# Optimization experiments

Measured on AMD Instinct MI355X. Metric: run time of the kernel, lower is better.

Reference implementation:

```python
import jax, jax.numpy as jnp
import numpy as np

B, L, F, H, HDE, E, V, MH, MW, TOUT = 64, 2, 512, 512, 512, 512, 94, 6, 40, 30
V2 = V + 2          # vocab + START/END + NULL slots
T = TOUT + 2        # decode steps
HW = MH * MW
START = V + 1
END = V + 1


def setup_inputs() -> dict:
    key = jax.random.key(0)
    ks = jax.random.split(key, 20)
    s = 0.05  # weight scale for numerical stability
    n = lambda k, shape: jax.random.normal(k, shape, jnp.float32) * s
    d = {}
    d['conv_f'] = jax.random.normal(ks[0], (B, F, MH, MW), jnp.float32)
    d['target'] = jax.random.randint(ks[1], (B, TOUT), 0, 95, dtype=jnp.int32)
    d['w_ih_en'] = n(ks[2], (L, 4 * H, F))
    d['w_hh_en'] = n(ks[3], (L, 4 * H, H))
    d['b_ih_en'] = n(ks[4], (L, 4 * H))
    d['b_hh_en'] = n(ks[5], (L, 4 * H))
    d['embed_w'] = n(ks[6], (V2, H))
    d['w_ih_de'] = n(ks[7], (L, 4 * HDE, H))
    d['w_hh_de'] = n(ks[8], (L, 4 * HDE, HDE))
    d['b_ih_de'] = n(ks[9], (L, 4 * HDE))
    d['b_hh_de'] = n(ks[10], (L, 4 * HDE))
    d['att_wh'] = n(ks[11], (E, HDE))
    d['att_bh'] = n(ks[12], (E,))
    d['att_conv_w'] = n(ks[13], (E, F, 3, 3))
    d['att_conv_b'] = n(ks[14], (E,))
    d['att_wv'] = n(ks[15], (1, E))
    d['att_bv'] = n(ks[16], (1,))
    d['out_w'] = n(ks[17], (V2, HDE + F))
    d['out_b'] = n(ks[18], (V2,))
    return d


def _lstm_cell(x, h, c, wih, whh, bih, bhh):
    # PyTorch gate order: i, f, g, o
    g = x @ wih.T + h @ whh.T + bih + bhh
    i, f, gg, o = jnp.split(g, 4, axis=-1)
    c_new = jax.nn.sigmoid(f) * c + jax.nn.sigmoid(i) * jnp.tanh(gg)
    h_new = jax.nn.sigmoid(o) * jnp.tanh(c_new)
    return h_new, c_new


def _forward(conv_f, target, w_ih_en, w_hh_en, b_ih_en, b_hh_en, embed_w,
             w_ih_de, w_hh_de, b_ih_de, b_hh_de, att_wh, att_bh,
             att_conv_w, att_conv_b, att_wv, att_bv, out_w, out_b):
    # ---- encoder: maxpool over full height, then 2-layer LSTM over width ----
    x_seq = jnp.max(conv_f, axis=2).transpose(2, 0, 1)  # [W, B, F]

    def enc_step(carry, xt):
        h, c = carry
        inp = xt
        hs, cs = [], []
        for l in range(L):
            hl, cl = _lstm_cell(inp, h[l], c[l], w_ih_en[l], w_hh_en[l],
                                b_ih_en[l], b_hh_en[l])
            inp = hl
            hs.append(hl); cs.append(cl)
        return (jnp.stack(hs), jnp.stack(cs)), inp

    z = jnp.zeros((L, B, H), conv_f.dtype)
    _, enc_out = jax.lax.scan(enc_step, (z, z), x_seq)
    holistic = enc_out[-1]  # [B, H]

    # ---- attention: conv_f embedding computed ONCE (invariant across steps) ----
    xe = jax.lax.conv_general_dilated(
        conv_f, att_conv_w, (1, 1), 'SAME',
        dimension_numbers=('NCHW', 'OIHW', 'NCHW')) + att_conv_b[None, :, None, None]
    x_em = xe.reshape(B, E, HW).transpose(0, 2, 1)       # [B, HW, E]
    cf_flat = conv_f.reshape(B, F, HW).transpose(0, 2, 1)  # [B, HW, F]

    # ---- decoder inputs: t=0 holistic, t>=1 embed(gt_with_start[:, t-1]) ----
    gt = jnp.concatenate(
        [jnp.full((B, 1), START, dtype=target.dtype), target], axis=1)  # [B, T-1]
    xs = jnp.concatenate([holistic[None], embed_w[gt.T]], axis=0)  # [T, B, H]

    def dec_step(carry, xt):
        h, c = carry
        inp = xt
        hs, cs = [], []
        for l in range(L):
            hl, cl = _lstm_cell(inp, h[l], c[l], w_ih_de[l], w_hh_de[l],
                                b_ih_de[l], b_hh_de[l])
            inp = hl
            hs.append(hl); cs.append(cl)
        hlast = inp  # [B, HDE]
        g_em = hlast @ att_wh.T + att_bh                    # [B, E]
        feat = jnp.tanh(x_em + g_em[:, None, :])            # [B, HW, E] (dropout=identity)
        e = feat @ att_wv[0] + att_bv[0]                    # [B, HW]
        alpha = jax.nn.softmax(e, axis=-1)
        att = jnp.einsum('bw,bwf->bf', alpha, cf_flat)      # [B, F]
        logits = jnp.concatenate([hlast, att], axis=-1) @ out_w.T + out_b
        scores = jax.nn.log_softmax(logits, axis=-1)        # [B, V2]
        return (jnp.stack(hs), jnp.stack(cs)), scores

    zd = jnp.zeros((B, HDE), conv_f.dtype)
    z0 = jnp.stack([zd] * L)
    _, out_tbv = jax.lax.scan(dec_step, (z0, z0), xs)  # [T, B, V2]
    out = out_tbv.transpose(1, 0, 2)                    # [B, T, V2]

    # ---- build l_target: [0, target..., 0] with first padding 0 -> END ----
    l_target = jnp.zeros((B, T), jnp.int32).at[:, 1:-1].set(target)
    j = jnp.argmax(l_target[:, 1:] == 0, axis=1) + 1  # first zero at col>=1 (always exists)
    l_target = l_target.at[jnp.arange(B), j].set(END)

    # ---- masked NLL loss ----
    lt = l_target.reshape(-1)
    nll = -out.reshape(-1, V2)[jnp.arange(B * T), lt]
    mask = (lt != 0).astype(out.dtype)
    return jnp.sum(nll * mask) / jnp.sum(mask)


def reference(conv_f, target, w_ih_en, w_hh_en, b_ih_en, b_hh_en, embed_w,
              w_ih_de, w_hh_de, b_ih_de, b_hh_de, att_wh, att_bh,
              att_conv_w, att_conv_b, att_wv, att_bv, out_w, out_b):
    return _forward(conv_f, target, w_ih_en, w_hh_en, b_ih_en, b_hh_en, embed_w,
                    w_ih_de, w_hh_de, b_ih_de, b_hh_de, att_wh, att_bh,
                    att_conv_w, att_conv_b, att_wv, att_bv, out_w, out_b)
```

## Files before the change

kernel.cpp:

```cpp
#include <hip/hip_runtime.h>

typedef __fp16 f16;
typedef __fp16 f16x4 __attribute__((ext_vector_type(4)));
typedef __fp16 f16x8 __attribute__((ext_vector_type(8)));
typedef float  f32x4 __attribute__((ext_vector_type(4)));
typedef unsigned long long ull;

#define DEV static __device__ __forceinline__

DEV f32x4 mfma16(f16x4 a, f16x4 b, f32x4 c) {
  return __builtin_amdgcn_mfma_f32_16x16x16f16(a, b, c, 0, 0, 0);
}
DEV f16x4 lo4(f16x8 v) { return __builtin_shufflevector(v, v, 0, 1, 2, 3); }
DEV f16x4 hi4(f16x8 v) { return __builtin_shufflevector(v, v, 4, 5, 6, 7); }
DEV float sigf(float x) { return 1.f / (1.f + __expf(-x)); }
DEV float tanh_(float x) { float e = __expf(2.f * x); return 1.f - 2.f / (e + 1.f); }

union U8 { float4 f4; float2 f2[2]; };
union H2 { unsigned u; f16 h[2]; };
union H4 { ull u; f16 h[4]; f16x4 v; };

#define HB 32768

DEV ull ldU(const ull* p) {
  return __hip_atomic_load(p, __ATOMIC_RELAXED, __HIP_MEMORY_SCOPE_AGENT);
}
DEV unsigned ldF(const unsigned* p) {
  return __hip_atomic_load(p, __ATOMIC_RELAXED, __HIP_MEMORY_SCOPE_AGENT);
}
DEV void stU32(unsigned* p, unsigned v) {
  __hip_atomic_store(p, v, __ATOMIC_RELAXED, __HIP_MEMORY_SCOPE_AGENT);
}
DEV void stU64(ull* p, ull v) {
  __hip_atomic_store(p, v, __ATOMIC_RELAXED, __HIP_MEMORY_SCOPE_AGENT);
}

DEV void wait8(const unsigned* line, unsigned tgt) {
  if (threadIdx.x < 8)
    while (ldF(line + threadIdx.x * 16) < tgt) {}
  __syncthreads();
}

DEV void signalDone(unsigned* line, int slot) {
  asm volatile("s_waitcnt vmcnt(0)" ::: "memory");
  __syncthreads();
  if (threadIdx.x == 0)
    __hip_atomic_fetch_add(line + slot * 16, 1u, __ATOMIC_RELAXED, __HIP_MEMORY_SCOPE_AGENT);
}

DEV void stageRow(const f16* __restrict__ s, f16* __restrict__ dstRow, int ch) {
  U8 u0, u1;
  u0.f4 = *(const float4*)s;
  u1.f4 = *(const float4*)(s + 8);
  *(float2*)(dstRow +  0 + ch * 4) = u0.f2[0];
  *(float2*)(dstRow + 16 + ch * 4) = u0.f2[1];
  *(float2*)(dstRow + 32 + ch * 4) = u1.f2[0];
  *(float2*)(dstRow + 48 + ch * 4) = u1.f2[1];
}

DEV void stageAp(const f16* __restrict__ rowSrc, f16 (*A)[64][72], int tid) {
  int ch = tid & 3;
  const f16* s = rowSrc + ch * 16;
#pragma unroll
  for (int c = 0; c < 8; ++c)
    stageRow(s + c * 64, &A[c][tid >> 2][0], ch);
}

DEV void stageAu(const ull* __restrict__ srcU, f16 (*A)[64][72], int tid) {
  int row = tid >> 2, ch = tid & 3;
  const ull* s = srcU + row * 128 + ch * 4;
#pragma unroll
  for (int c = 0; c < 8; ++c) {
    ull d0 = ldU(s + c * 16 + 0);
    ull d1 = ldU(s + c * 16 + 1);
    ull d2 = ldU(s + c * 16 + 2);
    ull d3 = ldU(s + c * 16 + 3);
    f16* d = &A[c][row][0];
    *(ull*)(d +  0 + ch * 4) = d0;
    *(ull*)(d + 16 + ch * 4) = d1;
    *(ull*)(d + 32 + ch * 4) = d2;
    *(ull*)(d + 48 + ch * 4) = d3;
  }
}

DEV void kloop32(const f16 (*Wt)[32][72], const f16 (*A)[64][72],
                 int mh, int ns, int m16, int g4, f32x4 acc[2]) {
#pragma unroll
  for (int c = 0; c < 8; ++c) {
#pragma unroll
    for (int half = 0; half < 2; ++half) {
      f16x8 bf = *(const f16x8*)&Wt[c][ns * 16 + m16][g4 * 16 + half * 8];
      f16x4 bl = lo4(bf), bh = hi4(bf);
#pragma unroll
      for (int mt = 0; mt < 2; ++mt) {
        f16x8 af = *(const f16x8*)&A[c][mh * 32 + mt * 16 + m16][g4 * 16 + half * 8];
        acc[mt] = mfma16(lo4(af), bl, acc[mt]);
        acc[mt] = mfma16(hi4(af), bh, acc[mt]);
      }
    }
  }
}

DEV void kloop64(const f16* Wg, const f16 (*A)[64][72],
                 int nsG, int m16, int g4, f32x4 acc[4]) {
#pragma unroll
  for (int c = 0; c < 8; ++c) {
#pragma unroll
    for (int half = 0; half < 2; ++half) {
      f16x8 bf = *(const f16x8*)&Wg[((size_t)(c * 64 + nsG * 16 + m16)) * 72 + g4 * 16 + half * 8];
      f16x4 bl = lo4(bf), bh = hi4(bf);
#pragma unroll
      for (int mt = 0; mt < 4; ++mt) {
        f16x8 af = *(const f16x8*)&A[c][mt * 16 + m16][g4 * 16 + half * 8];
        acc[mt] = mfma16(lo4(af), bl, acc[mt]);
        acc[mt] = mfma16(hi4(af), bh, acc[mt]);
      }
    }
  }
}

DEV void convTile(char* smem, int tile, const f16* __restrict__ cfT,
                  const f16* __restrict__ wc9, const float* __restrict__ cb,
                  f16* __restrict__ xemH) {
  f16 (*At)[40] = (f16(*)[40])smem;
  f16 (*Bt)[40] = (f16(*)[40])(smem + 19200);
  const int t = threadIdx.x, lane = t & 63, w = t >> 6;
  const int b = tile >> 2, eb = (tile & 3) * 128;
  const int m16 = lane & 15, g4 = lane >> 4;
  f32x4 acc[15][2] = {};

  for (int kr = 0; kr < 9; ++kr) {
    int dh = kr / 3 - 1, dw = kr % 3 - 1;
    for (int f0 = 0; f0 < 512; f0 += 32) {
      __syncthreads();
      if (t < 240) {
        int hh = t / 40 + dh, ww = t % 40 + dw;
        if (hh >= 0 && hh < 6 && ww >= 0 && ww < 40) {
          const f16* s = cfT + ((size_t)(b * 240 + hh * 40 + ww) * 512 + f0);
          U8 u0, u1, u2, u3;
          u0.f4 = *(const float4*)s;        u1.f4 = *(const float4*)(s + 8);
          u2.f4 = *(const float4*)(s + 16); u3.f4 = *(const float4*)(s + 24);
          *(float2*)&At[t][ 0] = u0.f2[0];
          *(float2*)&At[t][ 8] = u0.f2[1];
          *(float2*)&At[t][16] = u1.f2[0];
          *(float2*)&At[t][24] = u1.f2[1];
          *(float2*)&At[t][ 4] = u2.f2[0];
          *(float2*)&At[t][12] = u2.f2[1];
          *(float2*)&At[t][20] = u3.f2[0];
          *(float2*)&At[t][28] = u3.f2[1];
        } else {
          float2 z = make_float2(0.f, 0.f);
          *(float2*)&At[t][ 0] = z; *(float2*)&At[t][ 8] = z;
          *(float2*)&At[t][16] = z; *(float2*)&At[t][24] = z;
          *(float2*)&At[t][ 4] = z; *(float2*)&At[t][12] = z;
          *(float2*)&At[t][20] = z; *(float2*)&At[t][28] = z;
        }
      }
      {
        int n = t >> 1, ch = t & 1;
        const f16* s = wc9 + (size_t)(eb + n) * 4608 + kr * 512 + f0 + ch * 16;
        U8 u0, u1;
        u0.f4 = *(const float4*)s; u1.f4 = *(const float4*)(s + 8);
        *(float2*)&Bt[n][ 0 + ch * 4] = u0.f2[0];
        *(float2*)&Bt[n][ 8 + ch * 4] = u0.f2[1];
        *(float2*)&Bt[n][16 + ch * 4] = u1.f2[0];
        *(float2*)&Bt[n][24 + ch * 4] = u1.f2[1];
      }
      __syncthreads();
      f16x8 b0 = *(const f16x8*)&Bt[w * 32 + m16][g4 * 8];
      f16x8 b1v = *(const f16x8*)&Bt[w * 32 + 16 + m16][g4 * 8];
      f16x4 b0l = lo4(b0), b0h = hi4(b0), b1l = lo4(b1v), b1h = hi4(b1v);
#pragma unroll
      for (int mt = 0; mt < 15; ++mt) {
        f16x8 af = *(const f16x8*)&At[mt * 16 + m16][g4 * 8];
        f16x4 al = lo4(af), ah = hi4(af);
        acc[mt][0] = mfma16(al, b0l, acc[mt][0]);
        acc[mt][1] = mfma16(al, b1l, acc[mt][1]);
        acc[mt][0] = mfma16(ah, b0h, acc[mt][0]);
        acc[mt][1] = mfma16(ah, b1h, acc[mt][1]);
      }
    }
  }
#pragma unroll
  for (int nt = 0; nt < 2; ++nt) {
    int e = eb + w * 32 + nt * 16 + m16;
    float bias = cb[e];
#pragma unroll
    for (int mt = 0; mt < 15; ++mt)
#pragma unroll
      for (int r = 0; r < 4; ++r) {
        int p = mt * 16 + g4 * 4 + r;
        xemH[((size_t)(b * 240 + p)) * 512 + e] = (f16)(acc[mt][nt][r] + bias);
      }
  }
}


__global__ void k_convW(const float* __restrict__ s0, const float* __restrict__ s1,
                        const float* __restrict__ s2, const float* __restrict__ s3,
                        f16* __restrict__ d0, f16* __restrict__ d1,
                        f16* __restrict__ d2, f16* __restrict__ d3) {
  int i = blockIdx.x * 256 + threadIdx.x;
  int sel = i >> 19, j = i & 524287;
  const float* s = sel == 0 ? s0 : sel == 1 ? s1 : sel == 2 ? s2 : s3;
  f16* d = sel == 0 ? d0 : sel == 1 ? d1 : sel == 2 ? d2 : d3;
  float4 v = ((const float4*)s)[j];
  f16x4 o = { (f16)v.x, (f16)v.y, (f16)v.z, (f16)v.w };
  *(f16x4*)(d + (size_t)j * 4) = o;
}

__global__ void k_convS(const float* __restrict__ awhS, const float* __restrict__ embS,
                        const float* __restrict__ outwS,
                        f16* __restrict__ awhD, f16* __restrict__ embD,
                        f16* __restrict__ outwD) {
  int i = blockIdx.x * 256 + threadIdx.x;
  const float* s; f16* d; int j;
  if (i < 65536) { s = awhS; d = awhD; j = i; }
  else if (i < 65536 + 12288) { s = embS; d = embD; j = i - 65536; }
  else if (i < 65536 + 12288 + 24576) { s = outwS; d = outwD; j = i - 65536 - 12288; }
  else return;
  float4 v = ((const float4*)s)[j];
  f16x4 o = { (f16)v.x, (f16)v.y, (f16)v.z, (f16)v.w };
  *(f16x4*)(d + (size_t)j * 4) = o;
}

__global__ __launch_bounds__(256) void k_wc9(const float* __restrict__ src, f16* __restrict__ dst) {
  __shared__ float s[4608];
  const int e = blockIdx.x, tid = threadIdx.x;
  for (int i = tid; i < 4608; i += 256) s[i] = src[(size_t)e * 4608 + i];
  __syncthreads();
  for (int j = tid; j < 4608; j += 256) {
    int rr = j >> 9, f = j & 511;
    dst[(size_t)e * 4608 + j] = (f16)s[f * 9 + rr];
  }
}

__global__ __launch_bounds__(256) void k_cfmx(
    const float* __restrict__ cf, f16* __restrict__ cfT, f16* __restrict__ xseq)
{
  __shared__ float sT[64][244];
  const int tid = threadIdx.x;
  const int f0 = blockIdx.x * 64, b = blockIdx.y;
  const float* src = cf + ((size_t)b * 512 + f0) * 240;
  for (int i = tid; i < 3840; i += 256) {
    float4 v = ((const float4*)src)[i];
    int fl = i / 60, pc = (i % 60) * 4;
    sT[fl][pc] = v.x; sT[fl][pc + 1] = v.y; sT[fl][pc + 2] = v.z; sT[fl][pc + 3] = v.w;
  }
  __syncthreads();
  if (tid < 240) {
    int p = tid;
    f16* drow = cfT + ((size_t)b * 240 + p) * 512 + f0;
#pragma unroll
    for (int j = 0; j < 8; ++j) {
      f16x8 o;
#pragma unroll
      for (int k = 0; k < 8; ++k) o[k] = (f16)sT[j * 8 + k][p];
      *(f16x8*)(drow + j * 8) = o;
    }
  }
  {
    int fl = tid >> 2, wq = tid & 3;
#pragma unroll
    for (int wi = 0; wi < 10; ++wi) {
      int w = wq * 10 + wi;
      float m = sT[fl][w];
#pragma unroll
      for (int h = 1; h < 6; ++h) m = fmaxf(m, sT[fl][h * 40 + w]);
      xseq[((size_t)w * 64 + b) * 512 + f0 + fl] = (f16)m;
    }
  }
}

__global__ void k_zero(unsigned* p0, unsigned* p1, unsigned* p2,
                       unsigned* p3, unsigned* p4, unsigned* p5) {
  int i = blockIdx.x * 256 + threadIdx.x;
  int sel = i >> 14, j = i & 16383;
  unsigned* p = sel == 0 ? p0 : sel == 1 ? p1 : sel == 2 ? p2 :
                sel == 3 ? p3 : sel == 4 ? p4 : p5;
  p[j] = 0;
}

__global__ __launch_bounds__(256) void k_gemmX(
    const f16* __restrict__ A, const f16* __restrict__ W,
    const float* __restrict__ b1, const float* __restrict__ b2,
    f16* __restrict__ C)
{
  __shared__ f16 At[64][72];
  __shared__ f16 Bt[64][72];
  const int t = threadIdx.x, lane = t & 63, g = t >> 6;
  f32x4 acc[4] = {};
  const int m16 = lane & 15, g4 = lane >> 4;
  const size_t arow0 = (size_t)blockIdx.x * 64;

  for (int k0 = 0; k0 < 512; k0 += 64) {
    __syncthreads();
    { int row = t >> 2, ch = t & 3;
      stageRow(A + (arow0 + row) * 512 + k0 + ch * 16, &At[row][0], ch); }
    { int row = t >> 2, ch = t & 3;
      stageRow(W + ((size_t)blockIdx.y * 64 + row) * 512 + k0 + ch * 16, &Bt[row][0], ch); }
    __syncthreads();
#pragma unroll
    for (int half = 0; half < 2; ++half) {
      f16x8 bf = *(const f16x8*)&Bt[g * 16 + m16][g4 * 16 + half * 8];
      f16x4 bl = lo4(bf), bh = hi4(bf);
#pragma unroll
      for (int mt = 0; mt < 4; ++mt) {
        f16x8 af = *(const f16x8*)&At[mt * 16 + m16][g4 * 16 + half * 8];
        acc[mt] = mfma16(lo4(af), bl, acc[mt]);
        acc[mt] = mfma16(hi4(af), bh, acc[mt]);
      }
    }
  }
  int e = blockIdx.y * 64 + g * 16 + m16;
  float bias = b1[e] + b2[e];
#pragma unroll
  for (int mt = 0; mt < 4; ++mt)
#pragma unroll
    for (int r = 0; r < 4; ++r)
      C[(arow0 + mt * 16 + g4 * 4 + r) * 2048 + e] = (f16)(acc[mt][r] + bias);
}

__global__ __launch_bounds__(256) void k_gemmXd(
    const f16* __restrict__ x_t0, const f16* __restrict__ emb, const int* __restrict__ tgt,
    const f16* __restrict__ W, const float* __restrict__ b1, const float* __restrict__ b2,
    f16* __restrict__ C)
{
  __shared__ f16 At[64][72];
  __shared__ f16 Bt[64][72];
  const int t = threadIdx.x, lane = t & 63, g = t >> 6;
  f32x4 acc[4] = {};
  const int m16 = lane & 15, g4 = lane >> 4;
  const int tt = blockIdx.x;
  const size_t arow0 = (size_t)tt * 64;
  const int row = t >> 2, ch = t & 3;
  const f16* rowSrc;
  if (tt == 0) rowSrc = x_t0 + (size_t)row * 512;
  else if (tt == 1) rowSrc = emb + (size_t)95 * 512;
  else { int tok = tgt[row * 30 + tt - 2]; rowSrc = emb + (size_t)tok * 512; }

  for (int k0 = 0; k0 < 512; k0 += 64) {
    __syncthreads();
    stageRow(rowSrc + k0 + ch * 16, &At[row][0], ch);
    stageRow(W + ((size_t)blockIdx.y * 64 + row) * 512 + k0 + ch * 16, &Bt[row][0], ch);
    __syncthreads();
#pragma unroll
    for (int half = 0; half < 2; ++half) {
      f16x8 bf = *(const f16x8*)&Bt[g * 16 + m16][g4 * 16 + half * 8];
      f16x4 bl = lo4(bf), bh = hi4(bf);
#pragma unroll
      for (int mt = 0; mt < 4; ++mt) {
        f16x8 af = *(const f16x8*)&At[mt * 16 + m16][g4 * 16 + half * 8];
        acc[mt] = mfma16(lo4(af), bl, acc[mt]);
        acc[mt] = mfma16(hi4(af), bh, acc[mt]);
      }
    }
  }
  int e = blockIdx.y * 64 + g * 16 + m16;
  float bias = b1[e] + b2[e];
#pragma unroll
  for (int mt = 0; mt < 4; ++mt)
#pragma unroll
    for (int r = 0; r < 4; ++r)
      C[(arow0 + mt * 16 + g4 * 4 + r) * 2048 + e] = (f16)(acc[mt][r] + bias);
}

__global__ __launch_bounds__(256, 1) void k_lstm(
    int T, int mode,
    const f16* __restrict__ G0, const f16* __restrict__ whh0,
    const f16* __restrict__ wih1, const f16* __restrict__ whh1,
    const float* __restrict__ bih1, const float* __restrict__ bhh1,
    f16* __restrict__ h0seq, f16* __restrict__ h1seq,
    unsigned* __restrict__ cnt,
    const f16* __restrict__ cfT, const f16* __restrict__ wc9,
    const float* __restrict__ cb, f16* __restrict__ xemH, int convBase,
    f16* __restrict__ X0de, const f16* __restrict__ wihD0,
    const float* __restrict__ bihD0, const float* __restrict__ bhhD0,
    const f16* __restrict__ emb, const int* __restrict__ tgt,
    const f16* __restrict__ awh, const float* __restrict__ gbias, f16* __restrict__ gAll)
{
  __shared__ __align__(16) char smem[147456];
  const int tid = threadIdx.x, lane = tid & 63, w = tid >> 6;
  const int m16 = lane & 15, g4 = lane >> 4;
  const int bid = blockIdx.x;

  if (bid < 32) {
    f16 (*sW)[64][72] = (f16(*)[64][72])smem;
    f16 (*sA)[64][72] = (f16(*)[64][72])(smem + 73728);
    float* sG = (float*)(smem + 73728);
    const int utile = bid;
    { int r = tid >> 2, ch = tid & 3;
      int grow = (r >> 4) * 512 + utile * 16 + (r & 15);
      for (int c = 0; c < 8; ++c)
        stageRow(whh0 + (size_t)grow * 512 + c * 64 + ch * 16, &sW[c][r][0], ch);
    }
    const int pb = tid >> 2, uq = tid & 3;
    float cst[4] = {0.f, 0.f, 0.f, 0.f};
    for (int t = 0; t < T; ++t) {
      if (t > 0) wait8(cnt + (size_t)(t - 1) * 128, 4);
      const f16* gpp = G0 + (size_t)(t * 64 + pb) * 2048 + utile * 16 + uq * 4;
      H4 gI, gF, gG, gO;
      gI.v = *(const f16x4*)(gpp);
      gF.v = *(const f16x4*)(gpp + 512);
      gG.v = *(const f16x4*)(gpp + 1024);
      gO.v = *(const f16x4*)(gpp + 1536);
      stageAu((const ull*)h0seq + (size_t)t * 8192, sA, tid);
      __syncthreads();
      f32x4 acc[4] = {};
      kloop64((const f16*)sW, sA, w, m16, g4, acc);
      __syncthreads();
#pragma unroll
      for (int mt = 0; mt < 4; ++mt)
#pragma unroll
        for (int r = 0; r < 4; ++r)
          sG[((size_t)w * 64 + mt * 16 + g4 * 4 + r) * 17 + m16] = acc[mt][r];
      __syncthreads();
      {
        H4 outp;
#pragma unroll
        for (int j = 0; j < 4; ++j) {
          int u = uq * 4 + j;
          float gi = sG[(0 * 64 + pb) * 17 + u] + (float)gI.h[j];
          float gf = sG[(1 * 64 + pb) * 17 + u] + (float)gF.h[j];
          float gg = sG[(2 * 64 + pb) * 17 + u] + (float)gG.h[j];
          float go = sG[(3 * 64 + pb) * 17 + u] + (float)gO.h[j];
          float cn = sigf(gf) * cst[j] + sigf(gi) * tanh_(gg);
          float hn = sigf(go) * tanh_(cn);
          cst[j] = cn;
          outp.h[j] = (f16)hn;
        }
        stU64((ull*)h0seq + (size_t)(t + 1) * 8192 + pb * 128 + utile * 4 + uq, outp.u);
      }
      signalDone(cnt + (size_t)t * 128, bid & 7);
    }
  } else if (bid < 96) {
    f16 (*sW2)[8][32][72] = (f16(*)[8][32][72])smem;
    f16 (*sA)[64][72] = (f16(*)[64][72])(smem + 73728);
    float* sG = (float*)(smem + 73728);
    const int utile = bid - 32;
    const int mh = w >> 1, ns = w & 1;
    { int mat = tid >> 7;
      int r = (tid >> 2) & 31, ch = tid & 3;
      int grow = (r >> 3) * 512 + utile * 8 + (r & 7);
      const f16* Wsrc = (mat == 0) ? wih1 : whh1;
      for (int c = 0; c < 8; ++c)
        stageRow(Wsrc + (size_t)grow * 512 + c * 64 + ch * 16, &sW2[mat][c][r][0], ch);
    }
    const int pb = tid >> 2, pup = tid & 3;
    float badd[4][2];
#pragma unroll
    for (int g = 0; g < 4; ++g)
#pragma unroll
      for (int j = 0; j < 2; ++j) {
        int rr = g * 512 + utile * 8 + pup * 2 + j;
        badd[g][j] = bih1[rr] + bhh1[rr];
      }
    float cst[2] = {0.f, 0.f};
    unsigned* line1 = cnt + (size_t)T * 128;
    for (int t = 0; t < T; ++t) {
      wait8(cnt + (size_t)t * 128, 4);
      stageAu((const ull*)h0seq + (size_t)(t + 1) * 8192, sA, tid);
      if (t > 0) wait8(line1 + (size_t)(t - 1) * 128, 8);
      else       __syncthreads();
      ull rg[8][4];
      { const ull* s1p = (const ull*)h1seq + (size_t)t * 8192 + (tid >> 2) * 128 + (tid & 3) * 4;
#pragma unroll
        for (int c = 0; c < 8; ++c)
#pragma unroll
          for (int q = 0; q < 4; ++q) rg[c][q] = ldU(s1p + c * 16 + q);
      }
      f32x4 acc[2] = {};
      kloop32(sW2[0], sA, mh, ns, m16, g4, acc);
      __syncthreads();
      { int row = tid >> 2, ch = tid & 3;
#pragma unroll
        for (int c = 0; c < 8; ++c) {
          f16* d = &sA[c][row][0];
          *(ull*)(d +  0 + ch * 4) = rg[c][0];
          *(ull*)(d + 16 + ch * 4) = rg[c][1];
          *(ull*)(d + 32 + ch * 4) = rg[c][2];
          *(ull*)(d + 48 + ch * 4) = rg[c][3];
        }
      }
      __syncthreads();
      kloop32(sW2[1], sA, mh, ns, m16, g4, acc);
      __syncthreads();
      { int nl = ns * 16 + m16;
#pragma unroll
        for (int mt = 0; mt < 2; ++mt)
#pragma unroll
          for (int r = 0; r < 4; ++r) {
            int b = mh * 32 + mt * 16 + g4 * 4 + r;
            sG[((nl >> 3) * 64 + b) * 9 + (nl & 7)] = acc[mt][r];
          }
      }
      __syncthreads();
      {
        H2 outp;
#pragma unroll
        for (int j = 0; j < 2; ++j) {
          int u = pup * 2 + j;
          float gi = sG[(0 * 64 + pb) * 9 + u] + badd[0][j];
          float gf = sG[(1 * 64 + pb) * 9 + u] + badd[1][j];
          float gg = sG[(2 * 64 + pb) * 9 + u] + badd[2][j];
          float go = sG[(3 * 64 + pb) * 9 + u] + badd[3][j];
          float cn = sigf(gf) * cst[j] + sigf(gi) * tanh_(gg);
          float hn = sigf(go) * tanh_(cn);
          cst[j] = cn;
          outp.h[j] = (f16)hn;
        }
        stU32((unsigned*)h1seq + (size_t)(t + 1) * 16384 + pb * 256 + utile * 4 + pup, outp.u);
      }
      signalDone(line1 + (size_t)t * 128, bid & 7);
    }
  } else if (bid < 224) {
    convTile(smem, convBase + bid - 96, cfT, wc9, cb, xemH);
  } else if (mode == 0) {
    const int rid = bid - 224;
    f16 (*sW)[64][72] = (f16(*)[64][72])smem;
    f16 (*sA)[64][72] = (f16(*)[64][72])(smem + 73728);
    { int r = tid >> 2, ch = tid & 3;
      for (int c = 0; c < 8; ++c)
        stageRow(wihD0 + (size_t)(rid * 64 + r) * 512 + c * 64 + ch * 16, &sW[c][r][0], ch);
    }
    const int e = rid * 64 + w * 16 + m16;
    const float bias_e = bihD0[e] + bhhD0[e];
    const int arow = tid >> 2;
    __syncthreads();
    for (int tt = 1; tt < 32; ++tt) {
      const f16* rowSrc = (tt == 1) ? emb + (size_t)95 * 512
                                    : emb + (size_t)tgt[arow * 30 + tt - 2] * 512;
      stageAp(rowSrc, sA, tid);
      __syncthreads();
      f32x4 acc[4] = {};
      kloop64((const f16*)sW, sA, w, m16, g4, acc);
      __syncthreads();
#pragma unroll
      for (int mt = 0; mt < 4; ++mt)
#pragma unroll
        for (int r = 0; r < 4; ++r)
          X0de[((size_t)tt * 64 + mt * 16 + g4 * 4 + r) * 2048 + e] = (f16)(acc[mt][r] + bias_e);
      __syncthreads();
    }
  } else {
    const int g = bid - 224;
    f16* sWg = (f16*)smem;
    f16 (*sA)[64][72] = (f16(*)[64][72])(smem + 73728);
    { int r = tid >> 2, ch = tid & 3;
      for (int c = 0; c < 8; ++c)
        stageRow(awh + (size_t)(g * 64 + r) * 512 + c * 64 + ch * 16,
                 sWg + ((size_t)(c * 64 + r)) * 72, ch);
    }
    const int e = g * 64 + w * 16 + m16;
    const float gb = gbias[e];
    __syncthreads();
    unsigned* line1 = cnt + (size_t)T * 128;
    for (int t = 0; t < T; ++t) {
      wait8(line1 + (size_t)t * 128, 8);
      stageAu((const ull*)h1seq + (size_t)(t + 1) * 8192, sA, tid);
      __syncthreads();
      f32x4 acc[4] = {};
      kloop64(sWg, sA, w, m16, g4, acc);
      __syncthreads();
#pragma unroll
      for (int mt = 0; mt < 4; ++mt)
#pragma unroll
        for (int r = 0; r < 4; ++r)
          gAll[(size_t)(t * 64 + mt * 16 + g4 * 4 + r) * 512 + e] = (f16)(acc[mt][r] + gb);
    }
  }
}


__global__ __launch_bounds__(256) void k_scoreAll(
    const f16* __restrict__ xemH, const f16* __restrict__ gAll,
    const float* __restrict__ wv, float* __restrict__ esc)
{
  __shared__ f16 sX[20][512];
  const int tid = threadIdx.x, lane = tid & 63, w = tid >> 6;
  const int tile = blockIdx.x, b = blockIdx.y;
  for (int i = tid; i < 20 * 64; i += 256) {
    int row = i >> 6, seg = i & 63;
    *(f16x8*)&sX[row][seg * 8] =
        *(const f16x8*)(xemH + ((size_t)(b * 240 + tile * 20 + row)) * 512 + seg * 8);
  }
  float w8[8];
  { const float4* wp = (const float4*)(wv + lane * 8);
    float4 wa = wp[0], wb = wp[1];
    w8[0] = wa.x; w8[1] = wa.y; w8[2] = wa.z; w8[3] = wa.w;
    w8[4] = wb.x; w8[5] = wb.y; w8[6] = wb.z; w8[7] = wb.w; }
  __syncthreads();
  for (int t = 0; t < 32; ++t) {
    f16x8 gv = *(const f16x8*)(gAll + ((size_t)(t * 64 + b)) * 512 + lane * 8);
    float g8[8];
#pragma unroll
    for (int j = 0; j < 8; ++j) g8[j] = (float)gv[j];
#pragma unroll
    for (int i = 0; i < 5; ++i) {
      int rr = i * 4 + w;
      f16x8 xv = *(const f16x8*)&sX[rr][lane * 8];
      float s = 0.f;
#pragma unroll
      for (int j = 0; j < 8; ++j) s += tanh_((float)xv[j] + g8[j]) * w8[j];
#pragma unroll
      for (int m = 32; m; m >>= 1) s += __shfl_xor(s, m);
      if (lane == 0) esc[((size_t)(t * 64 + b)) * 240 + tile * 20 + rr] = s;
    }
  }
}

__global__ __launch_bounds__(256) void k_smctx(
    const float* __restrict__ esc, const f16* __restrict__ cfT,
    const f16* __restrict__ h1seq, f16* __restrict__ ctx)
{
  __shared__ float aAl[8][240];
  const int tid = threadIdx.x, lane = tid & 63, w = tid >> 6;
  const int tq = blockIdx.x, b = blockIdx.y;
  for (int half = 0; half < 2; ++half) {
    int tt = w + half * 4;
    int t = tq * 8 + tt;
    const float* er = esc + ((size_t)(t * 64 + b)) * 240;
    float v[4];
    float mx = -1e30f;
#pragma unroll
    for (int q = 0; q < 4; ++q) {
      int p = lane + q * 64;
      v[q] = (p < 240) ? er[p] : -1e30f;
      mx = fmaxf(mx, v[q]);
    }
#pragma unroll
    for (int m = 32; m; m >>= 1) mx = fmaxf(mx, __shfl_xor(mx, m));
    float sum = 0.f;
#pragma unroll
    for (int q = 0; q < 4; ++q) { v[q] = __expf(v[q] - mx); sum += v[q]; }
#pragma unroll
    for (int m = 32; m; m >>= 1) sum += __shfl_xor(sum, m);
    float inv = 1.f / sum;
#pragma unroll
    for (int q = 0; q < 4; ++q) {
      int p = lane + q * 64;
      if (p < 240) aAl[tt][p] = v[q] * inv;
    }
  }
  __syncthreads();
  float acc[8][2] = {};
  const f16* cb = cfT + (size_t)b * 240 * 512;
  for (int p = 0; p < 240; ++p) {
    H2 cw; cw.u = *(const unsigned*)(cb + (size_t)p * 512 + tid * 2);
    float c0 = (float)cw.h[0], c1 = (float)cw.h[1];
#pragma unroll
    for (int tt = 0; tt < 8; ++tt) {
      float a = aAl[tt][p];
      acc[tt][0] += a * c0;
      acc[tt][1] += a * c1;
    }
  }
#pragma unroll
  for (int tt = 0; tt < 8; ++tt) {
    int t = tq * 8 + tt;
    size_t r = (size_t)(t * 64 + b);
    H2 o; o.h[0] = (f16)acc[tt][0]; o.h[1] = (f16)acc[tt][1];
    *(unsigned*)(ctx + r * 1024 + 512 + tid * 2) = o.u;
    *(unsigned*)(ctx + r * 1024 + tid * 2) =
        *(const unsigned*)(h1seq + (size_t)(t + 1) * HB + b * 512 + tid * 2);
  }
}

__global__ __launch_bounds__(256) void k_gemmL(
    const f16* __restrict__ A, const f16* __restrict__ W,
    const float* __restrict__ bias, float* __restrict__ C)
{
  __shared__ f16 At[64][72];
  __shared__ f16 Bt[64][72];
  const int t = threadIdx.x, lane = t & 63, g = t >> 6;
  f32x4 acc[4] = {};
  const int m16 = lane & 15, g4 = lane >> 4;
  const size_t arow0 = (size_t)blockIdx.x * 64;

  for (int k0 = 0; k0 < 1024; k0 += 64) {
    __syncthreads();
    { int row = t >> 2, ch = t & 3;
      stageRow(A + (arow0 + row) * 1024 + k0 + ch * 16, &At[row][0], ch); }
    { int row = t >> 2, ch = t & 3;
      stageRow(W + ((size_t)(blockIdx.y * 64 + row)) * 1024 + k0 + ch * 16, &Bt[row][0], ch); }
    __syncthreads();
#pragma unroll
    for (int half = 0; half < 2; ++half) {
      f16x8 bf = *(const f16x8*)&Bt[g * 16 + m16][g4 * 16 + half * 8];
      f16x4 bl = lo4(bf), bh = hi4(bf);
#pragma unroll
      for (int mt = 0; mt < 4; ++mt) {
        f16x8 af = *(const f16x8*)&At[mt * 16 + m16][g4 * 16 + half * 8];
        acc[mt] = mfma16(lo4(af), bl, acc[mt]);
        acc[mt] = mfma16(hi4(af), bh, acc[mt]);
      }
    }
  }
  int e = blockIdx.y * 64 + g * 16 + m16;
  if (e < 96) {
    float be = bias[e];
#pragma unroll
    for (int mt = 0; mt < 4; ++mt)
#pragma unroll
      for (int r = 0; r < 4; ++r)
        C[(arow0 + mt * 16 + g4 * 4 + r) * 96 + e] = acc[mt][r] + be;
  }
}

__global__ void k_nllloss(const float* __restrict__ lgt, const int* __restrict__ target,
                          float* __restrict__ out) {
  __shared__ int ltg[2048];
  __shared__ float sa[256], sb[256];
  int tid = threadIdx.x;
  if (tid < 64) {
    int b = tid;
    int row[32];
    row[0] = 0;
    for (int t = 1; t <= 30; ++t) row[t] = target[b * 30 + t - 1];
    row[31] = 0;
    int j = 1;
    while (row[j] != 0) ++j;
    row[j] = 95;
    for (int t = 0; t < 32; ++t) ltg[b * 32 + t] = row[t];
  }
  __syncthreads();
  float a = 0.f, m = 0.f;
  for (int r = tid; r < 2048; r += 256) {
    int t = r >> 6, b = r & 63;
    int tok = ltg[b * 32 + t];
    if (tok != 0) {
      const float* row = lgt + (size_t)r * 96;
      float mx = -1e30f;
      for (int j = 0; j < 96; ++j) mx = fmaxf(mx, row[j]);
      float s = 0.f;
      for (int j = 0; j < 96; ++j) s += __expf(row[j] - mx);
      a += mx + __logf(s) - row[tok];
      m += 1.f;
    }
  }
  sa[tid] = a; sb[tid] = m; __syncthreads();
  for (int s = 128; s; s >>= 1) { if (tid < s) { sa[tid] += sa[tid + s]; sb[tid] += sb[tid + s]; } __syncthreads(); }
  if (tid == 0) out[0] = sa[0] / sb[0];
}


extern "C" void kernel_launch(void* const* d_in, const int* in_sizes, int n_in,
                              void* d_out, int out_size, void* d_ws, size_t ws_size,
                              hipStream_t stream) {
  (void)in_sizes; (void)n_in; (void)out_size; (void)ws_size;
  const float* conv_f = (const float*)d_in[0];
  const int*   target = (const int*)d_in[1];
  const float* wih_en = (const float*)d_in[2];
  const float* whh_en = (const float*)d_in[3];
  const float* bih_en = (const float*)d_in[4];
  const float* bhh_en = (const float*)d_in[5];
  const float* embed  = (const float*)d_in[6];
  const float* wih_de = (const float*)d_in[7];
  const float* whh_de = (const float*)d_in[8];
  const float* bih_de = (const float*)d_in[9];
  const float* bhh_de = (const float*)d_in[10];
  const float* att_wh = (const float*)d_in[11];
  const float* att_bh = (const float*)d_in[12];
  const float* att_cw = (const float*)d_in[13];
  const float* att_cb = (const float*)d_in[14];
  const float* att_wv = (const float*)d_in[15];
  const float* out_w  = (const float*)d_in[17];
  const float* out_b  = (const float*)d_in[18];
  float* out = (float*)d_out;

  size_t o = 0;
  char* base = (char*)d_ws;
  auto take = [&](size_t bytes) -> void* {
    void* p = base + o;
    o += (bytes + 255) & ~(size_t)255;
    return p;
  };
  const size_t WSZ = (size_t)2048 * 512;
  f16* wihEn = (f16*)take(2 * WSZ * 2);
  f16* whhEn = (f16*)take(2 * WSZ * 2);
  f16* wihDe = (f16*)take(2 * WSZ * 2);
  f16* whhDe = (f16*)take(2 * WSZ * 2);
  f16* awh   = (f16*)take((size_t)512 * 512 * 2);
  f16* emb   = (f16*)take((size_t)96 * 512 * 2);
  f16* wc9   = (f16*)take((size_t)512 * 4608 * 2);
  f16* cfT   = (f16*)take((size_t)64 * 240 * 512 * 2);
  f16* xseq  = (f16*)take((size_t)40 * 64 * 512 * 2);
  f16* xemH  = (f16*)take((size_t)64 * 240 * 512 * 2);
  f16* outwH = (f16*)take((size_t)128 * 1024 * 2);
  f16* X0en  = (f16*)take((size_t)2560 * 2048 * 2);
  f16* X0de  = (f16*)take((size_t)2048 * 2048 * 2);
  f16* h0seqE = (f16*)take((size_t)41 * HB * 2);
  f16* h1seqE = (f16*)take((size_t)41 * HB * 2);
  f16* h0seqD = (f16*)take((size_t)33 * HB * 2);
  f16* h1seqD = (f16*)take((size_t)33 * HB * 2);
  f16* gAll   = (f16*)take((size_t)2048 * 512 * 2);
  unsigned* cntE = (unsigned*)take(65536);
  unsigned* cntD = (unsigned*)take(65536);
  float* escAll = (float*)X0en;
  float* lgtAll = (float*)((char*)X0en + 4194304);
  f16*   ctxAll = X0de;

  k_convW<<<8192, 256, 0, stream>>>(wih_en, whh_en, wih_de, whh_de,
                                    wihEn, whhEn, wihDe, whhDe);
  k_convS<<<400, 256, 0, stream>>>(att_wh, embed, out_w, awh, emb, outwH);
  k_wc9<<<512, 256, 0, stream>>>(att_cw, wc9);
  k_cfmx<<<dim3(8, 64), 256, 0, stream>>>(conv_f, cfT, xseq);
  k_zero<<<384, 256, 0, stream>>>((unsigned*)h0seqE, (unsigned*)h1seqE,
                                  (unsigned*)h0seqD, (unsigned*)h1seqD, cntE, cntD);

  k_gemmX<<<dim3(40, 32), 256, 0, stream>>>(xseq, wihEn, bih_en, bhh_en, X0en);
  k_lstm<<<256, 256, 0, stream>>>(40, 0, X0en, whhEn, wihEn + WSZ, whhEn + WSZ,
                                  bih_en + 2048, bhh_en + 2048, h0seqE, h1seqE, cntE,
                                  cfT, wc9, att_cb, xemH, 0,
                                  X0de, wihDe, bih_de, bhh_de, emb, target,
                                  nullptr, nullptr, nullptr);

  k_gemmXd<<<dim3(1, 32), 256, 0, stream>>>(h1seqE + (size_t)40 * HB, emb, target,
                                            wihDe, bih_de, bhh_de, X0de);
  k_lstm<<<232, 256, 0, stream>>>(32, 1, X0de, whhDe, wihDe + WSZ, whhDe + WSZ,
                                  bih_de + 2048, bhh_de + 2048, h0seqD, h1seqD, cntD,
                                  cfT, wc9, att_cb, xemH, 128,
                                  nullptr, nullptr, nullptr, nullptr, emb, target,
                                  awh, att_bh, gAll);

  k_scoreAll<<<dim3(12, 64), 256, 0, stream>>>(xemH, gAll, att_wv, escAll);
  k_smctx<<<dim3(4, 64), 256, 0, stream>>>(escAll, cfT, h1seqD, ctxAll);
  k_gemmL<<<dim3(32, 2), 256, 0, stream>>>(ctxAll, outwH, out_b, lgtAll);
  k_nllloss<<<1, 256, 0, stream>>>(lgtAll, target, out);
}
```

Baseline: 849.7 us.

## Merge prep kernels, fold decoder t0 gemm into LSTM, fuse logits with NLL

The four weight-conversion and zeroing kernels become one k_prep launch. The t=0 decoder input GEMM moves into the decoder LSTM kernel's attention blocks, which signal a counter that the recurrent blocks wait on. The logit GEMM is fused with the per-row log-softmax NLL, and the mask count is computed from the targets directly. The goal is fewer launches and no round-trip of the logits through global memory, at the cost of extra in-kernel synchronisation and a mostly serial per-row softmax.

```diff
diff --git a/kernel.cpp b/kernel.cpp
--- a/kernel.cpp
+++ b/kernel.cpp
@@ -195,43 +195,52 @@
   }
 }
 
-
-__global__ void k_convW(const float* __restrict__ s0, const float* __restrict__ s1,
-                        const float* __restrict__ s2, const float* __restrict__ s3,
-                        f16* __restrict__ d0, f16* __restrict__ d1,
-                        f16* __restrict__ d2, f16* __restrict__ d3) {
-  int i = blockIdx.x * 256 + threadIdx.x;
-  int sel = i >> 19, j = i & 524287;
-  const float* s = sel == 0 ? s0 : sel == 1 ? s1 : sel == 2 ? s2 : s3;
-  f16* d = sel == 0 ? d0 : sel == 1 ? d1 : sel == 2 ? d2 : d3;
-  float4 v = ((const float4*)s)[j];
-  f16x4 o = { (f16)v.x, (f16)v.y, (f16)v.z, (f16)v.w };
-  *(f16x4*)(d + (size_t)j * 4) = o;
-}
-
-__global__ void k_convS(const float* __restrict__ awhS, const float* __restrict__ embS,
-                        const float* __restrict__ outwS,
-                        f16* __restrict__ awhD, f16* __restrict__ embD,
-                        f16* __restrict__ outwD) {
-  int i = blockIdx.x * 256 + threadIdx.x;
-  const float* s; f16* d; int j;
-  if (i < 65536) { s = awhS; d = awhD; j = i; }
-  else if (i < 65536 + 12288) { s = embS; d = embD; j = i - 65536; }
-  else if (i < 65536 + 12288 + 24576) { s = outwS; d = outwD; j = i - 65536 - 12288; }
-  else return;
-  float4 v = ((const float4*)s)[j];
-  f16x4 o = { (f16)v.x, (f16)v.y, (f16)v.z, (f16)v.w };
-  *(f16x4*)(d + (size_t)j * 4) = o;
-}
-
-__global__ __launch_bounds__(256) void k_wc9(const float* __restrict__ src, f16* __restrict__ dst) {
-  __shared__ float s[4608];
-  const int e = blockIdx.x, tid = threadIdx.x;
-  for (int i = tid; i < 4608; i += 256) s[i] = src[(size_t)e * 4608 + i];
-  __syncthreads();
-  for (int j = tid; j < 4608; j += 256) {
-    int rr = j >> 9, f = j & 511;
-    dst[(size_t)e * 4608 + j] = (f16)s[f * 9 + rr];
+__global__ __launch_bounds__(256) void k_prep(
+    const float* __restrict__ att_cw, f16* __restrict__ wc9,
+    const float* __restrict__ s0, const float* __restrict__ s1,
+    const float* __restrict__ s2, const float* __restrict__ s3,
+    f16* __restrict__ d0, f16* __restrict__ d1,
+    f16* __restrict__ d2, f16* __restrict__ d3,
+    const float* __restrict__ awhS, const float* __restrict__ embS,
+    const float* __restrict__ outwS,
+    f16* __restrict__ awhD, f16* __restrict__ embD, f16* __restrict__ outwD,
+    unsigned* __restrict__ z0, unsigned* __restrict__ z1, unsigned* __restrict__ z2,
+    unsigned* __restrict__ z3, unsigned* __restrict__ z4, unsigned* __restrict__ z5)
+{
+  const int bid = blockIdx.x, tid = threadIdx.x;
+  if (bid < 512) {
+    __shared__ float s[4608];
+    const int e = bid;
+    for (int i = tid; i < 4608; i += 256) s[i] = att_cw[(size_t)e * 4608 + i];
+    __syncthreads();
+    for (int j = tid; j < 4608; j += 256) {
+      int rr = j >> 9, f = j & 511;
+      wc9[(size_t)e * 4608 + j] = (f16)s[f * 9 + rr];
+    }
+  } else if (bid < 8704) {
+    int i = (bid - 512) * 256 + tid;
+    int sel = i >> 19, j = i & 524287;
+    const float* s = sel == 0 ? s0 : sel == 1 ? s1 : sel == 2 ? s2 : s3;
+    f16* d = sel == 0 ? d0 : sel == 1 ? d1 : sel == 2 ? d2 : d3;
+    float4 v = ((const float4*)s)[j];
+    f16x4 o = { (f16)v.x, (f16)v.y, (f16)v.z, (f16)v.w };
+    *(f16x4*)(d + (size_t)j * 4) = o;
+  } else if (bid < 9104) {
+    int i = (bid - 8704) * 256 + tid;
+    const float* s; f16* d; int j;
+    if (i < 65536) { s = awhS; d = awhD; j = i; }
+    else if (i < 65536 + 12288) { s = embS; d = embD; j = i - 65536; }
+    else if (i < 65536 + 12288 + 24576) { s = outwS; d = outwD; j = i - 65536 - 12288; }
+    else return;
+    float4 v = ((const float4*)s)[j];
+    f16x4 o = { (f16)v.x, (f16)v.y, (f16)v.z, (f16)v.w };
+    *(f16x4*)(d + (size_t)j * 4) = o;
+  } else {
+    int i = (bid - 9104) * 256 + tid;
+    int sel = i >> 14, j = i & 16383;
+    unsigned* p = sel == 0 ? z0 : sel == 1 ? z1 : sel == 2 ? z2 :
+                  sel == 3 ? z3 : sel == 4 ? z4 : z5;
+    p[j] = 0;
   }
 }
 
@@ -272,15 +281,6 @@
   }
 }
 
-__global__ void k_zero(unsigned* p0, unsigned* p1, unsigned* p2,
-                       unsigned* p3, unsigned* p4, unsigned* p5) {
-  int i = blockIdx.x * 256 + threadIdx.x;
-  int sel = i >> 14, j = i & 16383;
-  unsigned* p = sel == 0 ? p0 : sel == 1 ? p1 : sel == 2 ? p2 :
-                sel == 3 ? p3 : sel == 4 ? p4 : p5;
-  p[j] = 0;
-}
-
 __global__ __launch_bounds__(256) void k_gemmX(
     const f16* __restrict__ A, const f16* __restrict__ W,
     const float* __restrict__ b1, const float* __restrict__ b2,
@@ -299,50 +299,6 @@
       stageRow(A + (arow0 + row) * 512 + k0 + ch * 16, &At[row][0], ch); }
     { int row = t >> 2, ch = t & 3;
       stageRow(W + ((size_t)blockIdx.y * 64 + row) * 512 + k0 + ch * 16, &Bt[row][0], ch); }
-    __syncthreads();
-#pragma unroll
-    for (int half = 0; half < 2; ++half) {
-      f16x8 bf = *(const f16x8*)&Bt[g * 16 + m16][g4 * 16 + half * 8];
-      f16x4 bl = lo4(bf), bh = hi4(bf);
-#pragma unroll
-      for (int mt = 0; mt < 4; ++mt) {
-        f16x8 af = *(const f16x8*)&At[mt * 16 + m16][g4 * 16 + half * 8];
-        acc[mt] = mfma16(lo4(af), bl, acc[mt]);
-        acc[mt] = mfma16(hi4(af), bh, acc[mt]);
-      }
-    }
-  }
-  int e = blockIdx.y * 64 + g * 16 + m16;
-  float bias = b1[e] + b2[e];
-#pragma unroll
-  for (int mt = 0; mt < 4; ++mt)
-#pragma unroll
-    for (int r = 0; r < 4; ++r)
-      C[(arow0 + mt * 16 + g4 * 4 + r) * 2048 + e] = (f16)(acc[mt][r] + bias);
-}
-
-__global__ __launch_bounds__(256) void k_gemmXd(
-    const f16* __restrict__ x_t0, const f16* __restrict__ emb, const int* __restrict__ tgt,
-    const f16* __restrict__ W, const float* __restrict__ b1, const float* __restrict__ b2,
-    f16* __restrict__ C)
-{
-  __shared__ f16 At[64][72];
-  __shared__ f16 Bt[64][72];
-  const int t = threadIdx.x, lane = t & 63, g = t >> 6;
-  f32x4 acc[4] = {};
-  const int m16 = lane & 15, g4 = lane >> 4;
-  const int tt = blockIdx.x;
-  const size_t arow0 = (size_t)tt * 64;
-  const int row = t >> 2, ch = t & 3;
-  const f16* rowSrc;
-  if (tt == 0) rowSrc = x_t0 + (size_t)row * 512;
-  else if (tt == 1) rowSrc = emb + (size_t)95 * 512;
-  else { int tok = tgt[row * 30 + tt - 2]; rowSrc = emb + (size_t)tok * 512; }
-
-  for (int k0 = 0; k0 < 512; k0 += 64) {
-    __syncthreads();
-    stageRow(rowSrc + k0 + ch * 16, &At[row][0], ch);
-    stageRow(W + ((size_t)blockIdx.y * 64 + row) * 512 + k0 + ch * 16, &Bt[row][0], ch);
     __syncthreads();
 #pragma unroll
     for (int half = 0; half < 2; ++half) {
@@ -377,6 +333,7 @@
     f16* __restrict__ X0de, const f16* __restrict__ wihD0,
     const float* __restrict__ bihD0, const float* __restrict__ bhhD0,
     const f16* __restrict__ emb, const int* __restrict__ tgt,
+    const f16* __restrict__ x_t0,
     const f16* __restrict__ awh, const float* __restrict__ gbias, f16* __restrict__ gAll)
 {
   __shared__ __align__(16) char smem[147456];
@@ -398,6 +355,7 @@
     float cst[4] = {0.f, 0.f, 0.f, 0.f};
     for (int t = 0; t < T; ++t) {
       if (t > 0) wait8(cnt + (size_t)(t - 1) * 128, 4);
+      else if (mode == 1) wait8(cnt + (size_t)(2 * T) * 128, 1);
       const f16* gpp = G0 + (size_t)(t * 64 + pb) * 2048 + utile * 16 + uq * 4;
       H4 gI, gF, gG, gO;
       gI.v = *(const f16x4*)(gpp);
@@ -546,6 +504,28 @@
     const int g = bid - 224;
     f16* sWg = (f16*)smem;
     f16 (*sA)[64][72] = (f16(*)[64][72])(smem + 73728);
+    stageAp(x_t0 + (size_t)(tid >> 2) * 512, sA, tid);
+    __syncthreads();
+    for (int q = 0; q < 4; ++q) {
+      const int rid = g * 4 + q;
+      { int r = tid >> 2, ch = tid & 3;
+        for (int c = 0; c < 8; ++c)
+          stageRow(wihD0 + (size_t)(rid * 64 + r) * 512 + c * 64 + ch * 16,
+                   sWg + ((size_t)(c * 64 + r)) * 72, ch);
+      }
+      __syncthreads();
+      f32x4 acc[4] = {};
+      kloop64(sWg, sA, w, m16, g4, acc);
+      const int e = rid * 64 + w * 16 + m16;
+      const float bias_e = bihD0[e] + bhhD0[e];
+#pragma unroll
+      for (int mt = 0; mt < 4; ++mt)
+#pragma unroll
+        for (int r = 0; r < 4; ++r)
+          X0de[((size_t)(mt * 16 + g4 * 4 + r)) * 2048 + e] = (f16)(acc[mt][r] + bias_e);
+      __syncthreads();
+    }
+    signalDone(cnt + (size_t)(2 * T) * 128, g);
     { int r = tid >> 2, ch = tid & 3;
       for (int c = 0; c < 8; ++c)
         stageRow(awh + (size_t)(g * 64 + r) * 512 + c * 64 + ch * 16,
@@ -666,77 +646,94 @@
   }
 }
 
-__global__ __launch_bounds__(256) void k_gemmL(
-    const f16* __restrict__ A, const f16* __restrict__ W,
-    const float* __restrict__ bias, float* __restrict__ C)
+__global__ __launch_bounds__(256) void k_logit(
+    const f16* __restrict__ A,
+    const f16* __restrict__ W,
+    const float* __restrict__ bias, const int* __restrict__ tgt,
+    float* __restrict__ nllb)
 {
   __shared__ f16 At[64][72];
-  __shared__ f16 Bt[64][72];
-  const int t = threadIdx.x, lane = t & 63, g = t >> 6;
-  f32x4 acc[4] = {};
+  __shared__ f16 Bt[2][64][72];
+  __shared__ float sL[64][100];
+  const int tid = threadIdx.x, lane = tid & 63, g = tid >> 6;
   const int m16 = lane & 15, g4 = lane >> 4;
-  const size_t arow0 = (size_t)blockIdx.x * 64;
+  const int t = blockIdx.x;
+  const size_t arow0 = (size_t)t * 64;
+  f32x4 acc[2][4] = {};
 
   for (int k0 = 0; k0 < 1024; k0 += 64) {
     __syncthreads();
-    { int row = t >> 2, ch = t & 3;
-      stageRow(A + (arow0 + row) * 1024 + k0 + ch * 16, &At[row][0], ch); }
-    { int row = t >> 2, ch = t & 3;
-      stageRow(W + ((size_t)(blockIdx.y * 64 + row)) * 1024 + k0 + ch * 16, &Bt[row][0], ch); }
+    { int row = tid >> 2, ch = tid & 3;
+      stageRow(A + (arow0 + row) * 1024 + k0 + ch * 16, &At[row][0], ch);
+      stageRow(W + (size_t)row * 1024 + k0 + ch * 16, &Bt[0][row][0], ch);
+      stageRow(W + (size_t)(64 + row) * 1024 + k0 + ch * 16, &Bt[1][row][0], ch); }
     __syncthreads();
 #pragma unroll
-    for (int half = 0; half < 2; ++half) {
-      f16x8 bf = *(const f16x8*)&Bt[g * 16 + m16][g4 * 16 + half * 8];
-      f16x4 bl = lo4(bf), bh = hi4(bf);
-#pragma unroll
-      for (int mt = 0; mt < 4; ++mt) {
-        f16x8 af = *(const f16x8*)&At[mt * 16 + m16][g4 * 16 + half * 8];
-        acc[mt] = mfma16(lo4(af), bl, acc[mt]);
-        acc[mt] = mfma16(hi4(af), bh, acc[mt]);
-      }
-    }
-  }
-  int e = blockIdx.y * 64 + g * 16 + m16;
-  if (e < 96) {
-    float be = bias[e];
-#pragma unroll
-    for (int mt = 0; mt < 4; ++mt)
-#pragma unroll
-      for (int r = 0; r < 4; ++r)
-        C[(arow0 + mt * 16 + g4 * 4 + r) * 96 + e] = acc[mt][r] + be;
-  }
-}
-
-__global__ void k_nllloss(const float* __restrict__ lgt, const int* __restrict__ target,
-                          float* __restrict__ out) {
-  __shared__ int ltg[2048];
+    for (int n2 = 0; n2 < 2; ++n2)
+#pragma unroll
+      for (int half = 0; half < 2; ++half) {
+        f16x8 bf = *(const f16x8*)&Bt[n2][g * 16 + m16][g4 * 16 + half * 8];
+        f16x4 bl = lo4(bf), bh = hi4(bf);
+#pragma unroll
+        for (int mt = 0; mt < 4; ++mt) {
+          f16x8 af = *(const f16x8*)&At[mt * 16 + m16][g4 * 16 + half * 8];
+          acc[n2][mt] = mfma16(lo4(af), bl, acc[n2][mt]);
+          acc[n2][mt] = mfma16(hi4(af), bh, acc[n2][mt]);
+        }
+      }
+  }
+  __syncthreads();
+#pragma unroll
+  for (int n2 = 0; n2 < 2; ++n2) {
+    int e = n2 * 64 + g * 16 + m16;
+    if (e < 96) {
+      float be = bias[e];
+#pragma unroll
+      for (int mt = 0; mt < 4; ++mt)
+#pragma unroll
+        for (int r = 0; r < 4; ++r)
+          sL[mt * 16 + g4 * 4 + r][e] = acc[n2][mt][r] + be;
+    }
+  }
+  __syncthreads();
+  if (tid < 64) {
+    int b = tid;
+    int jj = 31;
+    for (int q = 1; q <= 30; ++q)
+      if (tgt[b * 30 + q - 1] == 0) { jj = q; break; }
+    int tok = (t == 0 || t == 31) ? 0 : tgt[b * 30 + t - 1];
+    if (t == jj) tok = 95;
+    float val = 0.f;
+    if (tok != 0) {
+      float mx = -1e30f;
+      for (int j = 0; j < 96; ++j) mx = fmaxf(mx, sL[b][j]);
+      float s = 0.f;
+      for (int j = 0; j < 96; ++j) s += __expf(sL[b][j] - mx);
+      val = mx + __logf(s) - sL[b][tok];
+    }
+    nllb[t * 64 + b] = val;
+  }
+}
+
+__global__ void k_loss(const float* __restrict__ nllb, const int* __restrict__ tgt,
+                       float* __restrict__ out) {
   __shared__ float sa[256], sb[256];
   int tid = threadIdx.x;
+  float a = 0.f, m = 0.f;
+  for (int i = tid; i < 2048; i += 256) a += nllb[i];
   if (tid < 64) {
     int b = tid;
-    int row[32];
-    row[0] = 0;
-    for (int t = 1; t <= 30; ++t) row[t] = target[b * 30 + t - 1];
-    row[31] = 0;
-    int j = 1;
-    while (row[j] != 0) ++j;
-    row[j] = 95;
-    for (int t = 0; t < 32; ++t) ltg[b * 32 + t] = row[t];
-  }
-  __syncthreads();
-  float a = 0.f, m = 0.f;
-  for (int r = tid; r < 2048; r += 256) {
-    int t = r >> 6, b = r & 63;
-    int tok = ltg[b * 32 + t];
-    if (tok != 0) {
-      const float* row = lgt + (size_t)r * 96;
-      float mx = -1e30f;
-      for (int j = 0; j < 96; ++j) mx = fmaxf(mx, row[j]);
-      float s = 0.f;
-      for (int j = 0; j < 96; ++j) s += __expf(row[j] - mx);
-      a += mx + __logf(s) - row[tok];
-      m += 1.f;
-    }
+    int jj = 31;
+    for (int q = 1; q <= 30; ++q)
+      if (tgt[b * 30 + q - 1] == 0) { jj = q; break; }
+    int cnt = 0;
+    for (int t = 1; t <= 30; ++t) {
+      int v = tgt[b * 30 + t - 1];
+      if (t == jj) v = 95;
+      if (v != 0) ++cnt;
+    }
+    if (jj == 31) ++cnt;
+    m = (float)cnt;
   }
   sa[tid] = a; sb[tid] = m; __syncthreads();
   for (int s = 128; s; s >>= 1) { if (tid < s) { sa[tid] += sa[tid + s]; sb[tid] += sb[tid + s]; } __syncthreads(); }
@@ -794,37 +791,36 @@
   f16* h0seqD = (f16*)take((size_t)33 * HB * 2);
   f16* h1seqD = (f16*)take((size_t)33 * HB * 2);
   f16* gAll   = (f16*)take((size_t)2048 * 512 * 2);
+  float* nllb = (float*)take((size_t)2048 * 4);
   unsigned* cntE = (unsigned*)take(65536);
   unsigned* cntD = (unsigned*)take(65536);
   float* escAll = (float*)X0en;
-  float* lgtAll = (float*)((char*)X0en + 4194304);
   f16*   ctxAll = X0de;
 
-  k_convW<<<8192, 256, 0, stream>>>(wih_en, whh_en, wih_de, whh_de,
-                                    wihEn, whhEn, wihDe, whhDe);
-  k_convS<<<400, 256, 0, stream>>>(att_wh, embed, out_w, awh, emb, outwH);
-  k_wc9<<<512, 256, 0, stream>>>(att_cw, wc9);
   k_cfmx<<<dim3(8, 64), 256, 0, stream>>>(conv_f, cfT, xseq);
-  k_zero<<<384, 256, 0, stream>>>((unsigned*)h0seqE, (unsigned*)h1seqE,
-                                  (unsigned*)h0seqD, (unsigned*)h1seqD, cntE, cntD);
+  k_prep<<<9488, 256, 0, stream>>>(att_cw, wc9,
+                                   wih_en, whh_en, wih_de, whh_de,
+                                   wihEn, whhEn, wihDe, whhDe,
+                                   att_wh, embed, out_w, awh, emb, outwH,
+                                   (unsigned*)h0seqE, (unsigned*)h1seqE,
+                                   (unsigned*)h0seqD, (unsigned*)h1seqD, cntE, cntD);
 
   k_gemmX<<<dim3(40, 32), 256, 0, stream>>>(xseq, wihEn, bih_en, bhh_en, X0en);
   k_lstm<<<256, 256, 0, stream>>>(40, 0, X0en, whhEn, wihEn + WSZ, whhEn + WSZ,
                                   bih_en + 2048, bhh_en + 2048, h0seqE, h1seqE, cntE,
                                   cfT, wc9, att_cb, xemH, 0,
                                   X0de, wihDe, bih_de, bhh_de, emb, target,
-                                  nullptr, nullptr, nullptr);
-
-  k_gemmXd<<<dim3(1, 32), 256, 0, stream>>>(h1seqE + (size_t)40 * HB, emb, target,
-                                            wihDe, bih_de, bhh_de, X0de);
+                                  nullptr, nullptr, nullptr, nullptr);
+
   k_lstm<<<232, 256, 0, stream>>>(32, 1, X0de, whhDe, wihDe + WSZ, whhDe + WSZ,
                                   bih_de + 2048, bhh_de + 2048, h0seqD, h1seqD, cntD,
                                   cfT, wc9, att_cb, xemH, 128,
-                                  nullptr, nullptr, nullptr, nullptr, emb, target,
+                                  X0de, wihDe, bih_de, bhh_de, emb, target,
+                                  h1seqE + (size_t)40 * HB,
                                   awh, att_bh, gAll);
 
   k_scoreAll<<<dim3(12, 64), 256, 0, stream>>>(xemH, gAll, att_wv, escAll);
   k_smctx<<<dim3(4, 64), 256, 0, stream>>>(escAll, cfT, h1seqD, ctxAll);
-  k_gemmL<<<dim3(32, 2), 256, 0, stream>>>(ctxAll, outwH, out_b, lgtAll);
-  k_nllloss<<<1, 256, 0, stream>>>(lgtAll, target, out);
-}
+  k_logit<<<32, 256, 0, stream>>>(ctxAll, outwH, out_b, target, nllb);
+  k_loss<<<1, 256, 0, stream>>>(nllb, target, out);
+}
```

After: 769.8 us (median of 2 runs). 9.4% less time.
